# Kernel optimization log

Hardware: AMD Instinct MI355X
Metric: run time of the kernel (lower is better)

Reference implementation:

```python
import jax, jax.numpy as jnp
import numpy as np

EPS = 1e-05


def setup_inputs() -> dict:
    key = jax.random.key(0)
    k1, k2 = jax.random.split(key)
    B, H, N, D = 4, 16, 4096, 128
    x = jax.random.normal(k1, (B, H, N, D), dtype=jnp.float32)
    # learned raw (non-skew) parameter; skew-symmetrized in reference
    S_raw = jax.random.normal(k2, (H, D, D), dtype=jnp.float32) * 0.05
    return {"x": x, "S_raw": S_raw}


def reference(x, S_raw):
    # x: (B, H, N, D); S_raw: (H, D, D)
    B, H, N, D = x.shape
    S = S_raw - jnp.swapaxes(S_raw, -1, -2)          # skew-symmetric (H, D, D)
    I = jnp.eye(D, dtype=x.dtype)
    A = (1.0 + EPS) * I + S                           # I + S + eps*I
    Bmat = I - S
    # rhs: (H, D, B*N) matching torch permute/reshape/transpose
    rhs = x.transpose(1, 3, 0, 2).reshape(H, D, B * N)
    y0 = jnp.linalg.solve(A, rhs)                     # batched solve over H
    y = Bmat @ y0                                     # (H, D, B*N)
    y = y.reshape(H, D, B, N).transpose(2, 0, 3, 1)   # (B, H, N, D)
    return y
```

## Files before the change

### kernel.cpp

```cpp
#include <hip/hip_runtime.h>
#include <stdint.h>

typedef __attribute__((ext_vector_type(4))) float floatx4;
typedef __attribute__((ext_vector_type(8))) short shortx8;
typedef __attribute__((ext_vector_type(2))) __bf16 bf16x2;

#define EPSF 1e-5f

#if defined(__has_builtin)
#if __has_builtin(__builtin_amdgcn_cvt_pk_bf16_f32)
#define HAVE_CVT_PK_BF16 1
#endif
#if __has_builtin(__builtin_amdgcn_rcpf)
#define HAVE_RCPF 1
#endif
#endif

__device__ __forceinline__ unsigned int pack2_bf16(float a, float b) {
#ifdef HAVE_CVT_PK_BF16
    bf16x2 r = __builtin_amdgcn_cvt_pk_bf16_f32(a, b);
    union { bf16x2 v; unsigned int u; } cv; cv.v = r; return cv.u;
#else
    unsigned int ua = __float_as_uint(a), ub = __float_as_uint(b);
    ua = (ua + 0x7fffu + ((ua >> 16) & 1u)) >> 16;
    ub = (ub + 0x7fffu + ((ub >> 16) & 1u)) & 0xffff0000u;
    return ub | ua;
#endif
}

__device__ __forceinline__ float fast_rcp(float x) {
#ifdef HAVE_RCPF
    return __builtin_amdgcn_rcpf(x);
#else
    return 1.0f / x;
#endif
}

__global__ __launch_bounds__(512) void cayley_invert(
    const float* __restrict__ S_raw, unsigned short* __restrict__ Mb)
{
    const int h  = blockIdx.x;
    const int t  = threadIdx.x;
    const int i  = t >> 2;
    const int s  = t & 3;
    const int j0 = s << 5;
    const float* Sr = S_raw + (size_t)h * 16384;

    float loc[32];
#pragma unroll
    for (int m = 0; m < 32; ++m) {
        const int j = j0 + m;
        float v = Sr[i * 128 + j] - Sr[j * 128 + i];
        if (j == i) v += 1.0f + EPSF;
        loc[m] = v;
    }

    __shared__ __align__(16) float rowbuf[2][128];
    __shared__ float dumbuf[2][128];

    if (i == 0) {
#pragma unroll
        for (int q = 0; q < 8; ++q) {
            floatx4 w;
            w[0] = loc[q*4+0]; w[1] = loc[q*4+1]; w[2] = loc[q*4+2]; w[3] = loc[q*4+3];
            if (q == 0 && s == 0) w[0] += 1.0f;
            *(floatx4*)(&rowbuf[0][j0 + q*4]) = w;
        }
    }
    if (s == 0) {
        float dv = loc[0];
        if (i == 0) dv -= 1.0f;
        dumbuf[0][i] = dv;
    }
    __syncthreads();

    for (int kb = 0; kb < 4; ++kb) {
#pragma unroll
        for (int kk = 0; kk < 32; ++kk) {
            const int cur = kk & 1;
            const int nxt = cur ^ 1;
            const int k   = (kb << 5) + kk;

            const float wk  = rowbuf[cur][k];
            const float dum = dumbuf[cur][i];
            const float akk = wk - 1.0f;
            const float de  = dum * fast_rcp(akk);

            floatx4 rv[8];
#pragma unroll
            for (int q = 0; q < 8; ++q)
                rv[q] = *(const floatx4*)(&rowbuf[cur][j0 + q*4]);

#pragma unroll
            for (int m = 0; m < 32; ++m)
                loc[m] = fmaf(-de, rv[m >> 2][m & 3], loc[m]);

            const int kn = k + 1;
            if (kn < 128) {
                const int sp   = (kk == 31) ? kb + 1 : kb;
                const int mloc = (kk == 31) ? 0 : kk + 1;
                const int qm   = mloc >> 2, em = mloc & 3;

                if (i == kn) {
#pragma unroll
                    for (int q = 0; q < 8; ++q) {
                        floatx4 w;
                        w[0] = loc[q*4+0]; w[1] = loc[q*4+1];
                        w[2] = loc[q*4+2]; w[3] = loc[q*4+3];
                        if (q == qm && s == sp) w[em] += 1.0f;
                        *(floatx4*)(&rowbuf[nxt][j0 + q*4]) = w;
                    }
                }
                if (s == sp) {
                    float dv = loc[mloc];
                    if (i == kn) dv -= 1.0f;
                    dumbuf[nxt][i] = dv;
                }
            }
            __syncthreads();
        }
    }

    unsigned short* dst = Mb + (size_t)h * 16384 + i * 128 + j0;
#pragma unroll
    for (int q = 0; q < 4; ++q) {
        union { shortx8 v; unsigned int u[4]; } cv;
#pragma unroll
        for (int p = 0; p < 4; ++p) {
            const int m = q*8 + p*2;
            const float v0 = (2.0f + EPSF) * loc[m]   - ((j0 + m   == i) ? 1.0f : 0.0f);
            const float v1 = (2.0f + EPSF) * loc[m+1] - ((j0 + m+1 == i) ? 1.0f : 0.0f);
            cv.u[p] = pack2_bf16(v0, v1);
        }
        *(shortx8*)(dst + q*8) = cv.v;
    }
}

__global__ __launch_bounds__(256) void cayley_apply(
    const float* __restrict__ x, const unsigned short* __restrict__ Mb,
    float* __restrict__ y)
{
    const int bid   = blockIdx.x;
    const int bh    = bid >> 5;
    const int ntile = bid & 31;
    const int h     = bh & 15;
    const int tid   = threadIdx.x;
    const int w     = tid >> 6;
    const int lane  = tid & 63;
    const int l15   = lane & 15;
    const int quad  = lane >> 4;

    __shared__ __align__(16) unsigned short Msh[128 * 136];

    {
        const unsigned short* Mg = Mb + (size_t)h * 16384;
#pragma unroll
        for (int it = 0; it < 8; ++it) {
            const int c   = tid + it * 256;
            const int row = c >> 4;
            const int cc  = (c & 15) * 8;
            const shortx8 v = *(const shortx8*)(Mg + row * 128 + cc);
            *(shortx8*)(&Msh[row * 136 + cc]) = v;
        }
    }
    __syncthreads();

    const size_t base = (size_t)bh * (4096 * 128);
    const int rowbase = ntile * 128 + w * 32;

    floatx4 acc[2][8];
#pragma unroll
    for (int mt = 0; mt < 2; ++mt)
#pragma unroll
        for (int ct = 0; ct < 8; ++ct) acc[mt][ct] = (floatx4)0.0f;

#pragma unroll
    for (int ks = 0; ks < 4; ++ks) {
        const int koff = ks * 32 + quad * 8;

        shortx8 xf[2];
#pragma unroll
        for (int mt = 0; mt < 2; ++mt) {
            const float* xp = x + base + (size_t)(rowbase + mt * 16 + l15) * 128 + koff;
            const floatx4 a = *(const floatx4*)xp;
            const floatx4 b = *(const floatx4*)(xp + 4);
            union { shortx8 v; unsigned int u[4]; } cv;
            cv.u[0] = pack2_bf16(a[0], a[1]);
            cv.u[1] = pack2_bf16(a[2], a[3]);
            cv.u[2] = pack2_bf16(b[0], b[1]);
            cv.u[3] = pack2_bf16(b[2], b[3]);
            xf[mt] = cv.v;
        }

#pragma unroll
        for (int ct = 0; ct < 8; ++ct) {
            const int d = ct * 16 + l15;
            const shortx8 mf = *(const shortx8*)(&Msh[d * 136 + koff]);
            acc[0][ct] = __builtin_amdgcn_mfma_f32_16x16x32_bf16(mf, xf[0], acc[0][ct], 0, 0, 0);
            acc[1][ct] = __builtin_amdgcn_mfma_f32_16x16x32_bf16(mf, xf[1], acc[1][ct], 0, 0, 0);
        }
    }

#pragma unroll
    for (int mt = 0; mt < 2; ++mt) {
        const int row = rowbase + mt * 16 + l15;
        float* yr = y + base + (size_t)row * 128;
#pragma unroll
        for (int ct = 0; ct < 8; ++ct)
            *(floatx4*)(yr + ct * 16 + quad * 4) = acc[mt][ct];
    }
}

extern "C" void kernel_launch(void* const* d_in, const int* in_sizes, int n_in,
                              void* d_out, int out_size, void* d_ws, size_t ws_size,
                              hipStream_t stream) {
    const float* x     = (const float*)d_in[0];
    const float* S_raw = (const float*)d_in[1];
    float* y = (float*)d_out;
    unsigned short* Mb = (unsigned short*)d_ws;

    cayley_invert<<<16, 512, 0, stream>>>(S_raw, Mb);
    cayley_apply<<<64 * 32, 256, 0, stream>>>(x, Mb, y);
}
```

Measured before the change: 320.1 us.

## Persist apply blocks over more rows with prefetch and LDS-staged nontemporal stores

Each apply block now covers 512 rows instead of 128, launching 512 blocks instead of 2048, so every block reuses the staged M matrix across four times as many rows. Each wave walks eight 16-row tiles and register-prefetches the next tile's x while the current tile's MFMAs run. Outputs go through an LDS transpose buffer so each store writes contiguous row segments, and those stores are nontemporal. The cost is less parallelism (two blocks per CU), more registers and LDS per block, and a serial dependency chain inside each wave.

```diff
diff --git a/kernel.cpp b/kernel.cpp
--- a/kernel.cpp
+++ b/kernel.cpp
@@ -140,17 +140,18 @@
     const float* __restrict__ x, const unsigned short* __restrict__ Mb,
     float* __restrict__ y)
 {
-    const int bid   = blockIdx.x;
-    const int bh    = bid >> 5;
-    const int ntile = bid & 31;
-    const int h     = bh & 15;
-    const int tid   = threadIdx.x;
-    const int w     = tid >> 6;
-    const int lane  = tid & 63;
-    const int l15   = lane & 15;
-    const int quad  = lane >> 4;
+    const int bid  = blockIdx.x;
+    const int bh   = bid >> 3;
+    const int g    = bid & 7;
+    const int h    = bh & 15;
+    const int tid  = threadIdx.x;
+    const int w    = tid >> 6;
+    const int lane = tid & 63;
+    const int l15  = lane & 15;
+    const int quad = lane >> 4;
 
     __shared__ __align__(16) unsigned short Msh[128 * 136];
+    __shared__ __align__(16) float obuf[4 * 16 * 68];
 
     {
         const unsigned short* Mg = Mb + (size_t)h * 16384;
@@ -159,55 +160,77 @@
             const int c   = tid + it * 256;
             const int row = c >> 4;
             const int cc  = (c & 15) * 8;
-            const shortx8 v = *(const shortx8*)(Mg + row * 128 + cc);
-            *(shortx8*)(&Msh[row * 136 + cc]) = v;
+            *(shortx8*)(&Msh[row * 136 + cc]) = *(const shortx8*)(Mg + row * 128 + cc);
         }
     }
     __syncthreads();
 
     const size_t base = (size_t)bh * (4096 * 128);
-    const int rowbase = ntile * 128 + w * 32;
-
-    floatx4 acc[2][8];
-#pragma unroll
-    for (int mt = 0; mt < 2; ++mt)
-#pragma unroll
-        for (int ct = 0; ct < 8; ++ct) acc[mt][ct] = (floatx4)0.0f;
-
+    const int row0    = g * 512 + w * 128;
+    const float* xw   = x + base + (size_t)(row0 + l15) * 128;
+    float* ob         = obuf + w * (16 * 68);
+
+    floatx4 xa[2][8];
 #pragma unroll
     for (int ks = 0; ks < 4; ++ks) {
-        const int koff = ks * 32 + quad * 8;
-
-        shortx8 xf[2];
-#pragma unroll
-        for (int mt = 0; mt < 2; ++mt) {
-            const float* xp = x + base + (size_t)(rowbase + mt * 16 + l15) * 128 + koff;
-            const floatx4 a = *(const floatx4*)xp;
-            const floatx4 b = *(const floatx4*)(xp + 4);
+        xa[0][ks*2+0] = *(const floatx4*)(xw + ks*32 + quad*8);
+        xa[0][ks*2+1] = *(const floatx4*)(xw + ks*32 + quad*8 + 4);
+    }
+
+#pragma unroll
+    for (int t = 0; t < 8; ++t) {
+        const int cur = t & 1, nxt = cur ^ 1;
+        if (t < 7) {
+            const float* xn = xw + (size_t)(t + 1) * (16 * 128);
+#pragma unroll
+            for (int ks = 0; ks < 4; ++ks) {
+                xa[nxt][ks*2+0] = *(const floatx4*)(xn + ks*32 + quad*8);
+                xa[nxt][ks*2+1] = *(const floatx4*)(xn + ks*32 + quad*8 + 4);
+            }
+        }
+
+        shortx8 xf[4];
+#pragma unroll
+        for (int ks = 0; ks < 4; ++ks) {
+            const floatx4 a = xa[cur][ks*2+0];
+            const floatx4 b = xa[cur][ks*2+1];
             union { shortx8 v; unsigned int u[4]; } cv;
             cv.u[0] = pack2_bf16(a[0], a[1]);
             cv.u[1] = pack2_bf16(a[2], a[3]);
             cv.u[2] = pack2_bf16(b[0], b[1]);
             cv.u[3] = pack2_bf16(b[2], b[3]);
-            xf[mt] = cv.v;
-        }
-
-#pragma unroll
-        for (int ct = 0; ct < 8; ++ct) {
-            const int d = ct * 16 + l15;
-            const shortx8 mf = *(const shortx8*)(&Msh[d * 136 + koff]);
-            acc[0][ct] = __builtin_amdgcn_mfma_f32_16x16x32_bf16(mf, xf[0], acc[0][ct], 0, 0, 0);
-            acc[1][ct] = __builtin_amdgcn_mfma_f32_16x16x32_bf16(mf, xf[1], acc[1][ct], 0, 0, 0);
-        }
-    }
-
-#pragma unroll
-    for (int mt = 0; mt < 2; ++mt) {
-        const int row = rowbase + mt * 16 + l15;
-        float* yr = y + base + (size_t)row * 128;
-#pragma unroll
-        for (int ct = 0; ct < 8; ++ct)
-            *(floatx4*)(yr + ct * 16 + quad * 4) = acc[mt][ct];
+            xf[ks] = cv.v;
+        }
+
+        floatx4 acc[8];
+#pragma unroll
+        for (int ct = 0; ct < 8; ++ct) acc[ct] = (floatx4)0.0f;
+
+#pragma unroll
+        for (int ks = 0; ks < 4; ++ks) {
+            const int ko = ks * 32 + quad * 8;
+#pragma unroll
+            for (int ct = 0; ct < 8; ++ct) {
+                const shortx8 mf = *(const shortx8*)(&Msh[(ct*16 + l15) * 136 + ko]);
+                acc[ct] = __builtin_amdgcn_mfma_f32_16x16x32_bf16(mf, xf[ks], acc[ct], 0, 0, 0);
+            }
+        }
+
+        float* yt = y + base + (size_t)(row0 + t * 16) * 128;
+#pragma unroll
+        for (int dh = 0; dh < 2; ++dh) {
+#pragma unroll
+            for (int c = 0; c < 4; ++c)
+                *(floatx4*)(&ob[l15 * 68 + c * 16 + quad * 4]) = acc[dh*4 + c];
+#pragma unroll
+            for (int j = 0; j < 4; ++j) {
+                const int f   = j * 256 + lane * 4;
+                const int r   = f >> 6;
+                const int col = f & 63;
+                const floatx4 v = *(const floatx4*)(&ob[r * 68 + col]);
+                __builtin_nontemporal_store(v, (floatx4*)(yt + (size_t)r * 128 + dh * 64 + col));
+            }
+        }
     }
 }
 
@@ -220,5 +243,5 @@
     unsigned short* Mb = (unsigned short*)d_ws;
 
     cayley_invert<<<16, 512, 0, stream>>>(S_raw, Mb);
-    cayley_apply<<<64 * 32, 256, 0, stream>>>(x, Mb, y);
-}
+    cayley_apply<<<64 * 8, 256, 0, stream>>>(x, Mb, y);
+}
```

New measurement: 319.3 us. About the same (-0.2%).
